# Kernel tuning notes

Measured on AMD Instinct MI355X. Metric: run time of the kernel, lower is better.

Reference implementation:

```python
import jax, jax.numpy as jnp
import numpy as np

B, L, D = 2, 2048, 1024
H, HD = 16, 64   # num_heads, head_dim
LD = 256         # mla latent dim


def setup_inputs() -> dict:
    key = jax.random.key(0)
    ks = jax.random.split(key, 6)
    s = lambda fan_in: 1.0 / np.sqrt(fan_in)
    x_bld = jax.random.normal(ks[0], (B, L, D), dtype=jnp.float32)
    Wq = jax.random.normal(ks[1], (D, H, HD), dtype=jnp.float32) * s(D)
    Wkv_down = jax.random.normal(ks[2], (D, LD), dtype=jnp.float32) * s(D)
    Wk_up = jax.random.normal(ks[3], (LD, H, HD), dtype=jnp.float32) * s(LD)
    Wv_up = jax.random.normal(ks[4], (LD, H, HD), dtype=jnp.float32) * s(LD)
    Wout = jax.random.normal(ks[5], (H, HD, D), dtype=jnp.float32) * s(H * HD)
    return {"x_bld": x_bld, "Wq": Wq, "Wkv_down": Wkv_down,
            "Wk_up": Wk_up, "Wv_up": Wv_up, "Wout": Wout}


def reference(x_bld, Wq, Wkv_down, Wk_up, Wv_up, Wout):
    # projections
    q_blhd = jnp.einsum('bld,dhk->blhk', x_bld, Wq)
    latent_bll = jnp.einsum('bld,dc->blc', x_bld, Wkv_down)   # [B,L,LD]
    k_blhd = jnp.einsum('blc,chk->blhk', latent_bll, Wk_up)
    v_blhd = jnp.einsum('blc,chk->blhk', latent_bll, Wv_up)
    # attention scores [B,H,L,L]
    attn = jnp.einsum('bqhd,bkhd->bhqk', q_blhd, k_blhd) / jnp.sqrt(
        jnp.asarray(HD, dtype=x_bld.dtype))
    # causal mask (no window)
    l = x_bld.shape[1]
    mask = (jnp.arange(l)[None, :] <= jnp.arange(l)[:, None])[None, None]
    neg_inf = jnp.finfo(attn.dtype).min
    attn = jax.nn.softmax(jnp.where(mask, attn, neg_inf), axis=-1)
    y_blhd = jnp.einsum('bhqk,bkhd->bqhd', attn, v_blhd)
    return jnp.einsum('bqhd,hdo->bqo', y_blhd, Wout)
```

## Files before the change

kernel.cpp:

```cpp
#include <hip/hip_runtime.h>
#include <hip/hip_bf16.h>

#define BB   2
#define LL   2048
#define DD   1024
#define HH   16
#define HDD  64
#define LDIM 256
#define MTOT (BB * LL)

using short8  = __attribute__((ext_vector_type(8))) short;
using floatx4 = __attribute__((ext_vector_type(4))) float;

static __device__ __forceinline__ unsigned short f2bf(float x) {
  __hip_bfloat16 h = __float2bfloat16(x);
  return *reinterpret_cast<unsigned short*>(&h);
}
static __device__ __forceinline__ unsigned int pk_bf16(float a, float b) {
  return (unsigned int)f2bf(a) | ((unsigned int)f2bf(b) << 16);
}
static __device__ __forceinline__ void load_lds16(const unsigned short* g,
                                                  unsigned short* l) {
  __builtin_amdgcn_global_load_lds(
      (const __attribute__((address_space(1))) unsigned int*)g,
      (__attribute__((address_space(3))) unsigned int*)l, 16, 0, 0);
}
template <int N>
static __device__ __forceinline__ void waitcnt_vm() {
  if constexpr (N == 0) asm volatile("s_waitcnt vmcnt(0)" ::: "memory");
  else if constexpr (N == 3) asm volatile("s_waitcnt vmcnt(3)" ::: "memory");
  else if constexpr (N == 4) asm volatile("s_waitcnt vmcnt(4)" ::: "memory");
  else if constexpr (N == 8) asm volatile("s_waitcnt vmcnt(8)" ::: "memory");
}

__global__ __launch_bounds__(256) void cast_bf16(const float* __restrict__ in,
                                                 unsigned short* __restrict__ out,
                                                 int n4) {
  const int i = (blockIdx.x * 256 + threadIdx.x);
  if (i < n4) {
    float4 v = ((const float4*)in)[i];
    ushort4 o;
    o.x = f2bf(v.x); o.y = f2bf(v.y); o.z = f2bf(v.z); o.w = f2bf(v.w);
    ((ushort4*)out)[i] = o;
  }
}

__global__ __launch_bounds__(256) void transpose_cast5(
    const float* __restrict__ Wq, const float* __restrict__ Wkv,
    const float* __restrict__ Wku, const float* __restrict__ Wvu,
    const float* __restrict__ Wo,
    unsigned short* __restrict__ WqT, unsigned short* __restrict__ WkvT,
    unsigned short* __restrict__ WkuT, unsigned short* __restrict__ WvuT,
    unsigned short* __restrict__ WoT) {
  const float* src; unsigned short* dst; int R, C;
  switch (blockIdx.z) {
    case 0:  src = Wq;  dst = WqT;  R = 1024; C = 1024; break;
    case 1:  src = Wkv; dst = WkvT; R = 1024; C = 256;  break;
    case 2:  src = Wku; dst = WkuT; R = 256;  C = 1024; break;
    case 3:  src = Wvu; dst = WvuT; R = 256;  C = 1024; break;
    default: src = Wo;  dst = WoT;  R = 1024; C = 1024; break;
  }
  if ((int)blockIdx.x * 32 >= C || (int)blockIdx.y * 32 >= R) return;

  __shared__ float tile[32][33];
  const int tx = threadIdx.x, ty = threadIdx.y;
#pragma unroll
  for (int i = 0; i < 4; ++i) {
    const int r = blockIdx.y * 32 + ty + i * 8;
    tile[ty + i * 8][tx] = src[(size_t)r * C + blockIdx.x * 32 + tx];
  }
  __syncthreads();
#pragma unroll
  for (int i = 0; i < 4; ++i) {
    const int c = blockIdx.x * 32 + ty + i * 8;
    dst[(size_t)c * R + blockIdx.y * 32 + tx] = f2bf(tile[tx][ty + i * 8]);
  }
}

template <int KIND, int BMT, int BNT>
__global__ __launch_bounds__(256) void gemm2(const unsigned short* __restrict__ A,
                                             const unsigned short* __restrict__ Bt0,
                                             const unsigned short* __restrict__ Bt1,
                                             void* __restrict__ C0,
                                             void* __restrict__ C1,
                                             int M, int N, int K, int nsplit) {
  constexpr int IM = BMT / 32, JN = BNT / 32;
  constexpr int NLD = BMT / 64 + BNT / 64;
  __shared__ __align__(16) unsigned short As[2 * BMT * 32];
  __shared__ __align__(16) unsigned short Bs[2 * BNT * 32];

  const int tid  = threadIdx.x;
  const int w    = tid >> 6;
  const int lane = tid & 63;
  const int lo   = lane & 15;
  const int g    = lane >> 4;
  const int wr   = w >> 1, wc = w & 1;
  const int row0  = blockIdx.y * BMT;
  const int col0g = blockIdx.x * BNT;
  const bool second = (col0g >= nsplit);
  const unsigned short* Btp = second ? Bt1 : Bt0;
  const int col0 = second ? col0g - nsplit : col0g;

  floatx4 acc[IM][JN];
#pragma unroll
  for (int i = 0; i < IM; ++i)
#pragma unroll
    for (int j = 0; j < JN; ++j) acc[i][j] = (floatx4){0.f, 0.f, 0.f, 0.f};

  const int sr = tid >> 2;
  const int sc = tid & 3;

  auto stage = [&](int buf, int k0) {
#pragma unroll
    for (int inst = 0; inst < BMT / 64; ++inst) {
      const int r  = inst * 64 + sr;
      const int cs = sc ^ ((r >> 1) & 3);
      load_lds16(A + (size_t)(row0 + r) * K + k0 + cs * 8,
                 As + buf * (BMT * 32) + inst * 2048 + w * 512);
    }
#pragma unroll
    for (int inst = 0; inst < BNT / 64; ++inst) {
      const int r  = inst * 64 + sr;
      const int cs = sc ^ ((r >> 1) & 3);
      load_lds16(Btp + (size_t)(col0 + r) * K + k0 + cs * 8,
                 Bs + buf * (BNT * 32) + inst * 2048 + w * 512);
    }
  };

  const int nk = K / 32;
  stage(0, 0);
  for (int it = 0; it < nk; ++it) {
    const int cur = it & 1;
    if (it + 1 < nk) {
      stage(cur ^ 1, (it + 1) * 32);
      waitcnt_vm<NLD>();
    } else {
      waitcnt_vm<0>();
    }
    asm volatile("s_barrier" ::: "memory");

    const unsigned short* Ac = As + cur * (BMT * 32);
    const unsigned short* Bc = Bs + cur * (BNT * 32);
    short8 af[IM], bf[JN];
#pragma unroll
    for (int i = 0; i < IM; ++i) {
      const int rm = (BMT / 2) * wr + 16 * i + lo;
      af[i] = *(const short8*)(Ac + rm * 32 + ((g ^ ((rm >> 1) & 3)) * 8));
    }
#pragma unroll
    for (int j = 0; j < JN; ++j) {
      const int rn = (BNT / 2) * wc + 16 * j + lo;
      bf[j] = *(const short8*)(Bc + rn * 32 + ((g ^ ((rn >> 1) & 3)) * 8));
    }
#pragma unroll
    for (int i = 0; i < IM; ++i)
#pragma unroll
      for (int j = 0; j < JN; ++j)
        acc[i][j] = __builtin_amdgcn_mfma_f32_16x16x32_bf16(af[i], bf[j], acc[i][j], 0, 0, 0);

    asm volatile("s_barrier" ::: "memory");
  }

#pragma unroll
  for (int i = 0; i < IM; ++i) {
    const int mbase = row0 + (BMT / 2) * wr + 16 * i + g * 4;
#pragma unroll
    for (int j = 0; j < JN; ++j) {
      const int nl = col0 + (BNT / 2) * wc + 16 * j + lo;
      const int bq = mbase >> 11, hh = nl >> 6, d = nl & 63;
      if (KIND == 2 && second) {
        const int l = mbase & 2047;
        uint2 o;
        o.x = pk_bf16(acc[i][j][0], acc[i][j][1]);
        o.y = pk_bf16(acc[i][j][2], acc[i][j][3]);
        *(uint2*)(&((unsigned short*)C1)[((size_t)(bq * HH + hh) * HDD + d) * LL + l]) = o;
      } else {
#pragma unroll
        for (int r = 0; r < 4; ++r) {
          const float v = acc[i][j][r];
          const int mm = mbase + r;
          const int l = mm & 2047;
          if (KIND == 0) {
            ((float*)C0)[(size_t)mm * N + nl] = v;
          } else if (KIND == 1) {
            if (!second)
              ((unsigned short*)C0)[((size_t)(bq * HH + hh) * LL + l) * HDD + d] = f2bf(v);
            else
              ((unsigned short*)C1)[(size_t)mm * LDIM + nl] = f2bf(v);
          } else {
            ((unsigned short*)C0)[((size_t)(bq * HH + hh) * LL + l) * HDD + d] = f2bf(v);
          }
        }
      }
    }
  }
}

#define SC2 0.18033688011112042f

__global__ __launch_bounds__(256) void flash_mfma5(const unsigned short* __restrict__ Qh,
                                                   const unsigned short* __restrict__ Kh,
                                                   const unsigned short* __restrict__ Vt,
                                                   unsigned short* __restrict__ y) {
  const int w    = threadIdx.x >> 6;
  const int lane = threadIdx.x & 63;
  const int lo   = lane & 15;
  const int g    = lane >> 4;
  const int pair = blockIdx.x;
  const int h    = blockIdx.y;
  const int b    = blockIdx.z;

  __shared__ __align__(16) unsigned short Ks[2 * 64 * 64];
  __shared__ __align__(16) unsigned short Vs[2 * 64 * 64];
  __shared__ __align__(16) unsigned short Pq[4][16 * 64];

  const size_t bh = (size_t)(b * HH + h);
  const unsigned short* Qp = Qh + bh * LL * HDD;
  const unsigned short* Kp = Kh + bh * LL * HDD;
  const unsigned short* Vp = Vt + bh * (size_t)HDD * LL;
  unsigned short* Pw = Pq[w];

  const int srow = lane >> 3;
  const int sch  = lane & 7;

  auto stage = [&](int buf, int k0) {
#pragma unroll
    for (int t = 0; t < 2; ++t) {
      const int rbase = w * 16 + t * 8;
      const int row   = rbase + srow;
      const int cs    = sch ^ (row & 7);
      load_lds16(Kp + (size_t)(k0 + row) * HDD + cs * 8, Ks + buf * 4096 + rbase * 64);
      load_lds16(Vp + (size_t)row * LL + k0 + cs * 8,    Vs + buf * 4096 + rbase * 64);
    }
  };

  auto process = [&](int qt) {
    const int q0 = qt * 64;
    const int qw = q0 + w * 16;
    const int ntiles = qt + 1;

    short8 qf0 = *(const short8*)(Qp + (size_t)(qw + lo) * HDD + g * 8);
    short8 qf1 = *(const short8*)(Qp + (size_t)(qw + lo) * HDD + 32 + g * 8);

    floatx4 ot[4];
#pragma unroll
    for (int ds = 0; ds < 4; ++ds) ot[ds] = (floatx4){0.f, 0.f, 0.f, 0.f};
    float lsum = 0.f;

    stage(0, 0);
    for (int it = 0; it < ntiles; ++it) {
      const int cur = it & 1;
      const int k0  = it * 64;
      if (it + 1 < ntiles) {
        stage(cur ^ 1, k0 + 64);
        waitcnt_vm<4>();
      } else {
        waitcnt_vm<0>();
      }
      asm volatile("s_barrier" ::: "memory");

      const unsigned short* Kc = Ks + cur * 4096;
      const unsigned short* Vc = Vs + cur * 4096;

      floatx4 st[4];
#pragma unroll
      for (int ks = 0; ks < 4; ++ks) {
        const int rm = ks * 16 + lo;
        short8 a0 = *(const short8*)(Kc + rm * 64 + ((g ^ (rm & 7)) * 8));
        short8 a1 = *(const short8*)(Kc + rm * 64 + (((4 + g) ^ (rm & 7)) * 8));
        floatx4 s = (floatx4){0.f, 0.f, 0.f, 0.f};
        s = __builtin_amdgcn_mfma_f32_16x16x32_bf16(a0, qf0, s, 0, 0, 0);
        s = __builtin_amdgcn_mfma_f32_16x16x32_bf16(a1, qf1, s, 0, 0, 0);
        st[ks] = s;
      }

      if (it + 1 < ntiles) {
#pragma unroll
        for (int ks = 0; ks < 4; ++ks) {
          float p[4];
#pragma unroll
          for (int r = 0; r < 4; ++r) {
            p[r] = __builtin_amdgcn_exp2f(st[ks][r] * SC2);
            lsum += p[r];
          }
          uint2 w2;
          w2.x = pk_bf16(p[0], p[1]);
          w2.y = pk_bf16(p[2], p[3]);
          *(uint2*)(Pw + lo * 64 + (((ks * 2 + (g >> 1)) ^ (lo & 7)) * 8) + (g & 1) * 4) = w2;
        }
      } else {
        const int qq = qw + lo;
#pragma unroll
        for (int ks = 0; ks < 4; ++ks) {
          float p[4];
#pragma unroll
          for (int r = 0; r < 4; ++r) {
            const int kk = k0 + ks * 16 + g * 4 + r;
            const float e = __builtin_amdgcn_exp2f(st[ks][r] * SC2);
            p[r] = (kk <= qq) ? e : 0.f;
            lsum += p[r];
          }
          uint2 w2;
          w2.x = pk_bf16(p[0], p[1]);
          w2.y = pk_bf16(p[2], p[3]);
          *(uint2*)(Pw + lo * 64 + (((ks * 2 + (g >> 1)) ^ (lo & 7)) * 8) + (g & 1) * 4) = w2;
        }
      }

      short8 pf0 = *(const short8*)(Pw + lo * 64 + ((g ^ (lo & 7)) * 8));
      short8 pf1 = *(const short8*)(Pw + lo * 64 + (((4 + g) ^ (lo & 7)) * 8));
#pragma unroll
      for (int ds = 0; ds < 4; ++ds) {
        const int rm = ds * 16 + lo;
        short8 v0 = *(const short8*)(Vc + rm * 64 + ((g ^ (rm & 7)) * 8));
        short8 v1 = *(const short8*)(Vc + rm * 64 + (((4 + g) ^ (rm & 7)) * 8));
        ot[ds] = __builtin_amdgcn_mfma_f32_16x16x32_bf16(v0, pf0, ot[ds], 0, 0, 0);
        ot[ds] = __builtin_amdgcn_mfma_f32_16x16x32_bf16(v1, pf1, ot[ds], 0, 0, 0);
      }

      asm volatile("s_barrier" ::: "memory");
    }

    float s = lsum;
    s += __shfl_xor(s, 16);
    s += __shfl_xor(s, 32);
    const float inv = 1.0f / s;
#pragma unroll
    for (int ds = 0; ds < 4; ++ds) {
      uint2 o;
      o.x = pk_bf16(ot[ds][0] * inv, ot[ds][1] * inv);
      o.y = pk_bf16(ot[ds][2] * inv, ot[ds][3] * inv);
      *(uint2*)(y + (size_t)(b * LL + qw + lo) * (HH * HDD) + h * HDD + ds * 16 + g * 4) = o;
    }
  };

  process(31 - pair);
  __syncthreads();
  process(pair);
}

extern "C" void kernel_launch(void* const* d_in, const int* in_sizes, int n_in,
                              void* d_out, int out_size, void* d_ws, size_t ws_size,
                              hipStream_t stream) {
  const float* x   = (const float*)d_in[0];
  const float* Wq  = (const float*)d_in[1];
  const float* Wkv = (const float*)d_in[2];
  const float* Wku = (const float*)d_in[3];
  const float* Wvu = (const float*)d_in[4];
  const float* Wo  = (const float*)d_in[5];
  float* out = (float*)d_out;

  unsigned short* xb     = (unsigned short*)d_ws;
  unsigned short* WqT    = xb + (size_t)MTOT * DD;
  unsigned short* WkvT   = WqT + 1024 * 1024;
  unsigned short* WkuT   = WkvT + 256 * 1024;
  unsigned short* WvuT   = WkuT + 1024 * 256;
  unsigned short* WoT    = WvuT + 1024 * 256;
  unsigned short* latent = WoT + 1024 * 1024;
  unsigned short* Qh     = latent + (size_t)MTOT * LDIM;
  unsigned short* Kh     = Qh + (size_t)MTOT * DD;
  unsigned short* Vt     = Kh + (size_t)MTOT * DD;
  unsigned short* y      = Vt + (size_t)MTOT * DD;

  cast_bf16<<<dim3(MTOT * DD / 1024), dim3(256), 0, stream>>>(x, xb, MTOT * DD / 4);
  transpose_cast5<<<dim3(32, 32, 5), dim3(32, 8), 0, stream>>>(
      Wq, Wkv, Wku, Wvu, Wo, WqT, WkvT, WkuT, WvuT, WoT);

  gemm2<1, 128, 128><<<dim3(1280 / 128, MTOT / 128), dim3(256), 0, stream>>>(
      xb, WqT, WkvT, Qh, latent, MTOT, 1280, DD, 1024);
  gemm2<2, 128, 128><<<dim3(2048 / 128, MTOT / 128), dim3(256), 0, stream>>>(
      latent, WkuT, WvuT, Kh, Vt, MTOT, 2048, LDIM, 1024);

  flash_mfma5<<<dim3(16, HH, BB), dim3(256), 0, stream>>>(Qh, Kh, Vt, y);

  gemm2<0, 128, 64><<<dim3(DD / 64, MTOT / 128), dim3(256), 0, stream>>>(
      y, WoT, nullptr, out, nullptr, MTOT, DD, DD, DD);
}
```

Baseline: 185.0 us.

## Share K/V tiles across paired query tiles in flash attention; reorder grids

```diff
diff --git a/kernel.cpp b/kernel.cpp
--- a/kernel.cpp
+++ b/kernel.cpp
@@ -28,7 +28,6 @@
 template <int N>
 static __device__ __forceinline__ void waitcnt_vm() {
   if constexpr (N == 0) asm volatile("s_waitcnt vmcnt(0)" ::: "memory");
-  else if constexpr (N == 3) asm volatile("s_waitcnt vmcnt(3)" ::: "memory");
   else if constexpr (N == 4) asm volatile("s_waitcnt vmcnt(4)" ::: "memory");
   else if constexpr (N == 8) asm volatile("s_waitcnt vmcnt(8)" ::: "memory");
 }
@@ -95,8 +94,8 @@
   const int lo   = lane & 15;
   const int g    = lane >> 4;
   const int wr   = w >> 1, wc = w & 1;
-  const int row0  = blockIdx.y * BMT;
-  const int col0g = blockIdx.x * BNT;
+  const int row0  = blockIdx.x * BMT;
+  const int col0g = blockIdx.y * BNT;
   const bool second = (col0g >= nsplit);
   const unsigned short* Btp = second ? Bt1 : Bt0;
   const int col0 = second ? col0g - nsplit : col0g;
@@ -198,7 +197,7 @@
 
 #define SC2 0.18033688011112042f
 
-__global__ __launch_bounds__(256) void flash_mfma5(const unsigned short* __restrict__ Qh,
+__global__ __launch_bounds__(256) void flash_mfma6(const unsigned short* __restrict__ Qh,
                                                    const unsigned short* __restrict__ Kh,
                                                    const unsigned short* __restrict__ Vt,
                                                    unsigned short* __restrict__ y) {
@@ -206,9 +205,11 @@
   const int lane = threadIdx.x & 63;
   const int lo   = lane & 15;
   const int g    = lane >> 4;
-  const int pair = blockIdx.x;
-  const int h    = blockIdx.y;
-  const int b    = blockIdx.z;
+  const int h    = blockIdx.x;
+  const int b    = blockIdx.y;
+  const int pair = blockIdx.z;
+  const int qtH  = 31 - pair;
+  const int qtL  = pair;
 
   __shared__ __align__(16) unsigned short Ks[2 * 64 * 64];
   __shared__ __align__(16) unsigned short Vs[2 * 64 * 64];
@@ -219,6 +220,22 @@
   const unsigned short* Kp = Kh + bh * LL * HDD;
   const unsigned short* Vp = Vt + bh * (size_t)HDD * LL;
   unsigned short* Pw = Pq[w];
+
+  const int qHw = qtH * 64 + w * 16;
+  const int qLw = qtL * 64 + w * 16;
+
+  short8 qfH0 = *(const short8*)(Qp + (size_t)(qHw + lo) * HDD + g * 8);
+  short8 qfH1 = *(const short8*)(Qp + (size_t)(qHw + lo) * HDD + 32 + g * 8);
+  short8 qfL0 = *(const short8*)(Qp + (size_t)(qLw + lo) * HDD + g * 8);
+  short8 qfL1 = *(const short8*)(Qp + (size_t)(qLw + lo) * HDD + 32 + g * 8);
+
+  floatx4 otH[4], otL[4];
+#pragma unroll
+  for (int ds = 0; ds < 4; ++ds) {
+    otH[ds] = (floatx4){0.f, 0.f, 0.f, 0.f};
+    otL[ds] = (floatx4){0.f, 0.f, 0.f, 0.f};
+  }
+  float lsumH = 0.f, lsumL = 0.f;
 
   const int srow = lane >> 3;
   const int sch  = lane & 7;
@@ -234,93 +251,88 @@
     }
   };
 
-  auto process = [&](int qt) {
-    const int q0 = qt * 64;
-    const int qw = q0 + w * 16;
-    const int ntiles = qt + 1;
-
-    short8 qf0 = *(const short8*)(Qp + (size_t)(qw + lo) * HDD + g * 8);
-    short8 qf1 = *(const short8*)(Qp + (size_t)(qw + lo) * HDD + 32 + g * 8);
-
-    floatx4 ot[4];
-#pragma unroll
-    for (int ds = 0; ds < 4; ++ds) ot[ds] = (floatx4){0.f, 0.f, 0.f, 0.f};
-    float lsum = 0.f;
-
-    stage(0, 0);
-    for (int it = 0; it < ntiles; ++it) {
-      const int cur = it & 1;
-      const int k0  = it * 64;
-      if (it + 1 < ntiles) {
-        stage(cur ^ 1, k0 + 64);
-        waitcnt_vm<4>();
-      } else {
-        waitcnt_vm<0>();
+  auto tile_qt = [&](const unsigned short* Kc, const unsigned short* Vc,
+                     short8 qf0, short8 qf1, floatx4* ot, float& lsum,
+                     int qw, int k0, bool masked) {
+    floatx4 st[4];
+#pragma unroll
+    for (int ks = 0; ks < 4; ++ks) {
+      const int rm = ks * 16 + lo;
+      short8 a0 = *(const short8*)(Kc + rm * 64 + ((g ^ (rm & 7)) * 8));
+      short8 a1 = *(const short8*)(Kc + rm * 64 + (((4 + g) ^ (rm & 7)) * 8));
+      floatx4 s = (floatx4){0.f, 0.f, 0.f, 0.f};
+      s = __builtin_amdgcn_mfma_f32_16x16x32_bf16(a0, qf0, s, 0, 0, 0);
+      s = __builtin_amdgcn_mfma_f32_16x16x32_bf16(a1, qf1, s, 0, 0, 0);
+      st[ks] = s;
+    }
+    if (!masked) {
+#pragma unroll
+      for (int ks = 0; ks < 4; ++ks) {
+        float p[4];
+#pragma unroll
+        for (int r = 0; r < 4; ++r) {
+          p[r] = __builtin_amdgcn_exp2f(st[ks][r] * SC2);
+          lsum += p[r];
+        }
+        uint2 w2;
+        w2.x = pk_bf16(p[0], p[1]);
+        w2.y = pk_bf16(p[2], p[3]);
+        *(uint2*)(Pw + lo * 64 + (((ks * 2 + (g >> 1)) ^ (lo & 7)) * 8) + (g & 1) * 4) = w2;
       }
-      asm volatile("s_barrier" ::: "memory");
-
-      const unsigned short* Kc = Ks + cur * 4096;
-      const unsigned short* Vc = Vs + cur * 4096;
-
-      floatx4 st[4];
+    } else {
+      const int qq = qw + lo;
 #pragma unroll
       for (int ks = 0; ks < 4; ++ks) {
-        const int rm = ks * 16 + lo;
-        short8 a0 = *(const short8*)(Kc + rm * 64 + ((g ^ (rm & 7)) * 8));
-        short8 a1 = *(const short8*)(Kc + rm * 64 + (((4 + g) ^ (rm & 7)) * 8));
-        floatx4 s = (floatx4){0.f, 0.f, 0.f, 0.f};
-        s = __builtin_amdgcn_mfma_f32_16x16x32_bf16(a0, qf0, s, 0, 0, 0);
-        s = __builtin_amdgcn_mfma_f32_16x16x32_bf16(a1, qf1, s, 0, 0, 0);
-        st[ks] = s;
+        float p[4];
+#pragma unroll
+        for (int r = 0; r < 4; ++r) {
+          const int kk = k0 + ks * 16 + g * 4 + r;
+          const float e = __builtin_amdgcn_exp2f(st[ks][r] * SC2);
+          p[r] = (kk <= qq) ? e : 0.f;
+          lsum += p[r];
+        }
+        uint2 w2;
+        w2.x = pk_bf16(p[0], p[1]);
+        w2.y = pk_bf16(p[2], p[3]);
+        *(uint2*)(Pw + lo * 64 + (((ks * 2 + (g >> 1)) ^ (lo & 7)) * 8) + (g & 1) * 4) = w2;
       }
-
-      if (it + 1 < ntiles) {
-#pragma unroll
-        for (int ks = 0; ks < 4; ++ks) {
-          float p[4];
-#pragma unroll
-          for (int r = 0; r < 4; ++r) {
-            p[r] = __builtin_amdgcn_exp2f(st[ks][r] * SC2);
-            lsum += p[r];
-          }
-          uint2 w2;
-          w2.x = pk_bf16(p[0], p[1]);
-          w2.y = pk_bf16(p[2], p[3]);
-          *(uint2*)(Pw + lo * 64 + (((ks * 2 + (g >> 1)) ^ (lo & 7)) * 8) + (g & 1) * 4) = w2;
-        }
-      } else {
-        const int qq = qw + lo;
-#pragma unroll
-        for (int ks = 0; ks < 4; ++ks) {
-          float p[4];
-#pragma unroll
-          for (int r = 0; r < 4; ++r) {
-            const int kk = k0 + ks * 16 + g * 4 + r;
-            const float e = __builtin_amdgcn_exp2f(st[ks][r] * SC2);
-            p[r] = (kk <= qq) ? e : 0.f;
-            lsum += p[r];
-          }
-          uint2 w2;
-          w2.x = pk_bf16(p[0], p[1]);
-          w2.y = pk_bf16(p[2], p[3]);
-          *(uint2*)(Pw + lo * 64 + (((ks * 2 + (g >> 1)) ^ (lo & 7)) * 8) + (g & 1) * 4) = w2;
-        }
-      }
-
-      short8 pf0 = *(const short8*)(Pw + lo * 64 + ((g ^ (lo & 7)) * 8));
-      short8 pf1 = *(const short8*)(Pw + lo * 64 + (((4 + g) ^ (lo & 7)) * 8));
-#pragma unroll
-      for (int ds = 0; ds < 4; ++ds) {
-        const int rm = ds * 16 + lo;
-        short8 v0 = *(const short8*)(Vc + rm * 64 + ((g ^ (rm & 7)) * 8));
-        short8 v1 = *(const short8*)(Vc + rm * 64 + (((4 + g) ^ (rm & 7)) * 8));
-        ot[ds] = __builtin_amdgcn_mfma_f32_16x16x32_bf16(v0, pf0, ot[ds], 0, 0, 0);
-        ot[ds] = __builtin_amdgcn_mfma_f32_16x16x32_bf16(v1, pf1, ot[ds], 0, 0, 0);
-      }
-
-      asm volatile("s_barrier" ::: "memory");
-    }
-
+    }
+    short8 pf0 = *(const short8*)(Pw + lo * 64 + ((g ^ (lo & 7)) * 8));
+    short8 pf1 = *(const short8*)(Pw + lo * 64 + (((4 + g) ^ (lo & 7)) * 8));
+#pragma unroll
+    for (int ds = 0; ds < 4; ++ds) {
+      const int rm = ds * 16 + lo;
+      short8 v0 = *(const short8*)(Vc + rm * 64 + ((g ^ (rm & 7)) * 8));
+      short8 v1 = *(const short8*)(Vc + rm * 64 + (((4 + g) ^ (rm & 7)) * 8));
+      ot[ds] = __builtin_amdgcn_mfma_f32_16x16x32_bf16(v0, pf0, ot[ds], 0, 0, 0);
+      ot[ds] = __builtin_amdgcn_mfma_f32_16x16x32_bf16(v1, pf1, ot[ds], 0, 0, 0);
+    }
+  };
+
+  const int ntiles = qtH + 1;
+  stage(0, 0);
+  for (int it = 0; it < ntiles; ++it) {
+    const int cur = it & 1;
+    const int k0  = it * 64;
+    if (it + 1 < ntiles) {
+      stage(cur ^ 1, k0 + 64);
+      waitcnt_vm<4>();
+    } else {
+      waitcnt_vm<0>();
+    }
+    asm volatile("s_barrier" ::: "memory");
+
+    const unsigned short* Kc = Ks + cur * 4096;
+    const unsigned short* Vc = Vs + cur * 4096;
+
+    tile_qt(Kc, Vc, qfH0, qfH1, otH, lsumH, qHw, k0, it == qtH);
+    if (it <= qtL)
+      tile_qt(Kc, Vc, qfL0, qfL1, otL, lsumL, qLw, k0, it == qtL);
+
+    asm volatile("s_barrier" ::: "memory");
+  }
+
+  auto finish = [&](floatx4* ot, float lsum, int qw) {
     float s = lsum;
     s += __shfl_xor(s, 16);
     s += __shfl_xor(s, 32);
@@ -333,10 +345,8 @@
       *(uint2*)(y + (size_t)(b * LL + qw + lo) * (HH * HDD) + h * HDD + ds * 16 + g * 4) = o;
     }
   };
-
-  process(31 - pair);
-  __syncthreads();
-  process(pair);
+  finish(otH, lsumH, qHw);
+  finish(otL, lsumL, qLw);
 }
 
 extern "C" void kernel_launch(void* const* d_in, const int* in_sizes, int n_in,
@@ -366,13 +376,13 @@
   transpose_cast5<<<dim3(32, 32, 5), dim3(32, 8), 0, stream>>>(
       Wq, Wkv, Wku, Wvu, Wo, WqT, WkvT, WkuT, WvuT, WoT);
 
-  gemm2<1, 128, 128><<<dim3(1280 / 128, MTOT / 128), dim3(256), 0, stream>>>(
+  gemm2<1, 128, 128><<<dim3(MTOT / 128, 1280 / 128), dim3(256), 0, stream>>>(
       xb, WqT, WkvT, Qh, latent, MTOT, 1280, DD, 1024);
-  gemm2<2, 128, 128><<<dim3(2048 / 128, MTOT / 128), dim3(256), 0, stream>>>(
+  gemm2<2, 128, 128><<<dim3(MTOT / 128, 2048 / 128), dim3(256), 0, stream>>>(
       latent, WkuT, WvuT, Kh, Vt, MTOT, 2048, LDIM, 1024);
 
-  flash_mfma5<<<dim3(16, HH, BB), dim3(256), 0, stream>>>(Qh, Kh, Vt, y);
-
-  gemm2<0, 128, 64><<<dim3(DD / 64, MTOT / 128), dim3(256), 0, stream>>>(
+  flash_mfma6<<<dim3(HH, BB, 16), dim3(256), 0, stream>>>(Qh, Kh, Vt, y);
+
+  gemm2<0, 128, 128><<<dim3(MTOT / 128, DD / 128), dim3(256), 0, stream>>>(
       y, WoT, nullptr, out, nullptr, MTOT, DD, DD, DD);
 }
```

Result: faster. 175.7 us (-5.0%).

## Split long causal query tiles across blocks with partial-sum merge kernel

Applied to the files above, without the earlier changes.

```diff
diff --git a/kernel.cpp b/kernel.cpp
--- a/kernel.cpp
+++ b/kernel.cpp
@@ -28,7 +28,6 @@
 template <int N>
 static __device__ __forceinline__ void waitcnt_vm() {
   if constexpr (N == 0) asm volatile("s_waitcnt vmcnt(0)" ::: "memory");
-  else if constexpr (N == 3) asm volatile("s_waitcnt vmcnt(3)" ::: "memory");
   else if constexpr (N == 4) asm volatile("s_waitcnt vmcnt(4)" ::: "memory");
   else if constexpr (N == 8) asm volatile("s_waitcnt vmcnt(8)" ::: "memory");
 }
@@ -95,8 +94,8 @@
   const int lo   = lane & 15;
   const int g    = lane >> 4;
   const int wr   = w >> 1, wc = w & 1;
-  const int row0  = blockIdx.y * BMT;
-  const int col0g = blockIdx.x * BNT;
+  const int row0  = blockIdx.x * BMT;
+  const int col0g = blockIdx.y * BNT;
   const bool second = (col0g >= nsplit);
   const unsigned short* Btp = second ? Bt1 : Bt0;
   const int col0 = second ? col0g - nsplit : col0g;
@@ -198,26 +197,28 @@
 
 #define SC2 0.18033688011112042f
 
-__global__ __launch_bounds__(256) void flash_mfma5(const unsigned short* __restrict__ Qh,
+__global__ __launch_bounds__(256) void flash_mfma7(const unsigned short* __restrict__ Qh,
                                                    const unsigned short* __restrict__ Kh,
                                                    const unsigned short* __restrict__ Vt,
-                                                   unsigned short* __restrict__ y) {
+                                                   unsigned short* __restrict__ y,
+                                                   float* __restrict__ Opart,
+                                                   float* __restrict__ lpart) {
   const int w    = threadIdx.x >> 6;
   const int lane = threadIdx.x & 63;
   const int lo   = lane & 15;
   const int g    = lane >> 4;
-  const int pair = blockIdx.x;
-  const int h    = blockIdx.y;
-  const int b    = blockIdx.z;
+  const int h    = blockIdx.x;
+  const int b    = blockIdx.y;
+  const int j    = blockIdx.z;
 
   __shared__ __align__(16) unsigned short Ks[2 * 64 * 64];
   __shared__ __align__(16) unsigned short Vs[2 * 64 * 64];
   __shared__ __align__(16) unsigned short Pq[4][16 * 64];
 
-  const size_t bh = (size_t)(b * HH + h);
-  const unsigned short* Qp = Qh + bh * LL * HDD;
-  const unsigned short* Kp = Kh + bh * LL * HDD;
-  const unsigned short* Vp = Vt + bh * (size_t)HDD * LL;
+  const int    bh = b * HH + h;
+  const unsigned short* Qp = Qh + (size_t)bh * LL * HDD;
+  const unsigned short* Kp = Kh + (size_t)bh * LL * HDD;
+  const unsigned short* Vp = Vt + (size_t)bh * HDD * LL;
   unsigned short* Pw = Pq[w];
 
   const int srow = lane >> 3;
@@ -234,11 +235,8 @@
     }
   };
 
-  auto process = [&](int qt) {
-    const int q0 = qt * 64;
-    const int qw = q0 + w * 16;
-    const int ntiles = qt + 1;
-
+  auto run_piece = [&](int qt, int it0, int it1, int piece, bool direct) {
+    const int qw = qt * 64 + w * 16;
     short8 qf0 = *(const short8*)(Qp + (size_t)(qw + lo) * HDD + g * 8);
     short8 qf1 = *(const short8*)(Qp + (size_t)(qw + lo) * HDD + 32 + g * 8);
 
@@ -247,11 +245,11 @@
     for (int ds = 0; ds < 4; ++ds) ot[ds] = (floatx4){0.f, 0.f, 0.f, 0.f};
     float lsum = 0.f;
 
-    stage(0, 0);
-    for (int it = 0; it < ntiles; ++it) {
-      const int cur = it & 1;
+    stage(0, it0 * 64);
+    for (int it = it0; it <= it1; ++it) {
+      const int cur = (it - it0) & 1;
       const int k0  = it * 64;
-      if (it + 1 < ntiles) {
+      if (it < it1) {
         stage(cur ^ 1, k0 + 64);
         waitcnt_vm<4>();
       } else {
@@ -273,8 +271,7 @@
         s = __builtin_amdgcn_mfma_f32_16x16x32_bf16(a1, qf1, s, 0, 0, 0);
         st[ks] = s;
       }
-
-      if (it + 1 < ntiles) {
+      if (it != qt) {
 #pragma unroll
         for (int ks = 0; ks < 4; ++ks) {
           float p[4];
@@ -306,7 +303,6 @@
           *(uint2*)(Pw + lo * 64 + (((ks * 2 + (g >> 1)) ^ (lo & 7)) * 8) + (g & 1) * 4) = w2;
         }
       }
-
       short8 pf0 = *(const short8*)(Pw + lo * 64 + ((g ^ (lo & 7)) * 8));
       short8 pf1 = *(const short8*)(Pw + lo * 64 + (((4 + g) ^ (lo & 7)) * 8));
 #pragma unroll
@@ -317,26 +313,70 @@
         ot[ds] = __builtin_amdgcn_mfma_f32_16x16x32_bf16(v0, pf0, ot[ds], 0, 0, 0);
         ot[ds] = __builtin_amdgcn_mfma_f32_16x16x32_bf16(v1, pf1, ot[ds], 0, 0, 0);
       }
-
       asm volatile("s_barrier" ::: "memory");
     }
 
     float s = lsum;
     s += __shfl_xor(s, 16);
     s += __shfl_xor(s, 32);
-    const float inv = 1.0f / s;
-#pragma unroll
-    for (int ds = 0; ds < 4; ++ds) {
-      uint2 o;
-      o.x = pk_bf16(ot[ds][0] * inv, ot[ds][1] * inv);
-      o.y = pk_bf16(ot[ds][2] * inv, ot[ds][3] * inv);
-      *(uint2*)(y + (size_t)(b * LL + qw + lo) * (HH * HDD) + h * HDD + ds * 16 + g * 4) = o;
+
+    if (direct) {
+      const float inv = 1.0f / s;
+#pragma unroll
+      for (int ds = 0; ds < 4; ++ds) {
+        uint2 o;
+        o.x = pk_bf16(ot[ds][0] * inv, ot[ds][1] * inv);
+        o.y = pk_bf16(ot[ds][2] * inv, ot[ds][3] * inv);
+        *(uint2*)(y + (size_t)(b * LL + qw + lo) * (HH * HDD) + h * HDD + ds * 16 + g * 4) = o;
+      }
+    } else {
+      const int slot = bh * 32 + (qt - 16) * 2 + piece;
+      float* Orow = Opart + ((size_t)slot * 64 + w * 16 + lo) * 64;
+#pragma unroll
+      for (int ds = 0; ds < 4; ++ds) {
+        float4 f = make_float4(ot[ds][0], ot[ds][1], ot[ds][2], ot[ds][3]);
+        *(float4*)(Orow + ds * 16 + g * 4) = f;
+      }
+      if (g == 0) lpart[(size_t)slot * 64 + w * 16 + lo] = s;
     }
   };
 
-  process(31 - pair);
-  __syncthreads();
-  process(pair);
+  if (j < 16) {
+    run_piece(j, 0, j, 0, true);
+    run_piece(31 - j, 16, 31 - j, 1, false);
+  } else {
+    run_piece(j, 0, 15, 0, false);
+  }
+}
+
+__global__ __launch_bounds__(256) void merge_flash(const float* __restrict__ Opart,
+                                                   const float* __restrict__ lpart,
+                                                   unsigned short* __restrict__ y) {
+  const int qt = 16 + blockIdx.x;
+  const int h  = blockIdx.y;
+  const int b  = blockIdx.z;
+  const int bh = b * HH + h;
+  const int t  = threadIdx.x;
+  const int q  = t >> 2;
+  const int dg = (t & 3) * 16;
+
+  const int s0 = bh * 32 + (qt - 16) * 2;
+  const float l = lpart[(size_t)s0 * 64 + q] + lpart[(size_t)(s0 + 1) * 64 + q];
+  const float inv = 1.0f / l;
+
+  const float* O0 = Opart + ((size_t)s0 * 64 + q) * 64 + dg;
+  const float* O1 = Opart + ((size_t)(s0 + 1) * 64 + q) * 64 + dg;
+  unsigned short* yp = y + (size_t)(b * LL + qt * 64 + q) * (HH * HDD) + h * HDD + dg;
+
+#pragma unroll
+  for (int i = 0; i < 4; ++i) {
+    float4 a = ((const float4*)O0)[i];
+    float4 c = ((const float4*)O1)[i];
+    uint2 o;
+    o.x = pk_bf16((a.x + c.x) * inv, (a.y + c.y) * inv);
+    o.y = pk_bf16((a.z + c.z) * inv, (a.w + c.w) * inv);
+    *(uint2*)(yp + i * 4) = o;
+  }
 }
 
 extern "C" void kernel_launch(void* const* d_in, const int* in_sizes, int n_in,
@@ -361,18 +401,21 @@
   unsigned short* Kh     = Qh + (size_t)MTOT * DD;
   unsigned short* Vt     = Kh + (size_t)MTOT * DD;
   unsigned short* y      = Vt + (size_t)MTOT * DD;
+  float* Opart = (float*)(y + (size_t)MTOT * DD);
+  float* lpart = Opart + (size_t)32 * 32 * 64 * 64;
 
   cast_bf16<<<dim3(MTOT * DD / 1024), dim3(256), 0, stream>>>(x, xb, MTOT * DD / 4);
   transpose_cast5<<<dim3(32, 32, 5), dim3(32, 8), 0, stream>>>(
       Wq, Wkv, Wku, Wvu, Wo, WqT, WkvT, WkuT, WvuT, WoT);
 
-  gemm2<1, 128, 128><<<dim3(1280 / 128, MTOT / 128), dim3(256), 0, stream>>>(
+  gemm2<1, 128, 128><<<dim3(MTOT / 128, 1280 / 128), dim3(256), 0, stream>>>(
       xb, WqT, WkvT, Qh, latent, MTOT, 1280, DD, 1024);
-  gemm2<2, 128, 128><<<dim3(2048 / 128, MTOT / 128), dim3(256), 0, stream>>>(
+  gemm2<2, 128, 128><<<dim3(MTOT / 128, 2048 / 128), dim3(256), 0, stream>>>(
       latent, WkuT, WvuT, Kh, Vt, MTOT, 2048, LDIM, 1024);
 
-  flash_mfma5<<<dim3(16, HH, BB), dim3(256), 0, stream>>>(Qh, Kh, Vt, y);
-
-  gemm2<0, 128, 64><<<dim3(DD / 64, MTOT / 128), dim3(256), 0, stream>>>(
+  flash_mfma7<<<dim3(HH, BB, 32), dim3(256), 0, stream>>>(Qh, Kh, Vt, y, Opart, lpart);
+  merge_flash<<<dim3(16, HH, BB), dim3(256), 0, stream>>>(Opart, lpart, y);
+
+  gemm2<0, 128, 128><<<dim3(MTOT / 128, DD / 128), dim3(256), 0, stream>>>(
       y, WoT, nullptr, out, nullptr, MTOT, DD, DD, DD);
 }
```

New measurement: 184.0 us. No clear change (-0.5%).
